# Kernel optimization log

Measured on AMD Instinct MI355X. Metric: run time of the kernel, lower is better.

The kernel has to match this reference:

```python
import jax, jax.numpy as jnp
import numpy as np

N = 32768
WORD_DIM, TAG_DIM, REL_DIM, MEM_DIM, AT_HID = 300, 20, 20, 150, 20
IN_LEAF = WORD_DIM + TAG_DIM                      # 320, input to leaf SimpleGRU
IN_NODE = WORD_DIM + MEM_DIM + REL_DIM + TAG_DIM  # 490, input to GRU_AT


def _build_tree(seed=0):
    rng = np.random.default_rng(seed)
    parent = np.zeros(N, np.int64)
    for i in range(1, N):
        parent[i] = rng.integers(max(0, i - 64), i)
    children = [[] for _ in range(N)]
    for i in range(1, N):
        children[parent[i]].append(i)
    # Edge schedule: parents in DECREASING index order, children ascending.
    # Since child index > parent index, all edges below a node fire before
    # the node itself is consumed as a child => same order as the Python
    # post-order recursion in the torch code.
    edges = []
    for p in range(N - 1, -1, -1):
        for c in children[p]:
            edges.append((p, c))
    edges = np.asarray(edges, np.int32)            # (N-1, 2)
    leaf_ids = np.asarray([i for i in range(N) if not children[i]], np.int32)
    return edges, leaf_ids


def setup_inputs() -> dict:
    key = jax.random.key(0)
    ks = jax.random.split(key, 16)
    s = 0.05
    edges, leaf_ids = _build_tree()
    return {
        "w_emb":  jax.random.normal(ks[0], (N, WORD_DIM), jnp.float32),
        "tag_emb": jax.random.normal(ks[1], (N, TAG_DIM), jnp.float32),
        "rel_emb": jax.random.normal(ks[2], (N, REL_DIM), jnp.float32),
        "leaf_h": jax.random.uniform(ks[3], (MEM_DIM,), jnp.float32),
        # leaf SimpleGRU: stacked [Wz,Wr,Wh], [Uz,Ur,Uh], combined bias bW+bU
        "leaf_W": jax.random.normal(ks[4], (3, MEM_DIM, IN_LEAF), jnp.float32) * s,
        "leaf_U": jax.random.normal(ks[5], (3, MEM_DIM, MEM_DIM), jnp.float32) * s,
        "leaf_b": jax.random.normal(ks[6], (3, MEM_DIM), jnp.float32) * s,
        # GRU_AT inner SimpleGRU
        "node_W": jax.random.normal(ks[7], (3, MEM_DIM, IN_NODE), jnp.float32) * s,
        "node_U": jax.random.normal(ks[8], (3, MEM_DIM, MEM_DIM), jnp.float32) * s,
        "node_b": jax.random.normal(ks[9], (3, MEM_DIM), jnp.float32) * s,
        # attention gate AT: sigmoid(Wa tanh(Wb x + bb) + ba)
        "at_Wb": jax.random.normal(ks[10], (AT_HID, IN_NODE), jnp.float32) * s,
        "at_bb": jax.random.normal(ks[11], (AT_HID,), jnp.float32) * s,
        "at_Wa": jax.random.normal(ks[12], (AT_HID,), jnp.float32) * s,
        "at_ba": jax.random.normal(ks[13], (), jnp.float32) * s,
        "edges": jnp.asarray(edges),
        "leaf_ids": jnp.asarray(leaf_ids),
    }


def _simple_gru(W, U, b, x, h):
    # z = s(Wz x + Uz h + b); r = s(...); ht = tanh(...)
    # h_new = r*h + (1-z)*ht   (as written in the torch code)
    pre = jnp.einsum('kmi,i->km', W, x) + jnp.einsum('kmn,n->km', U, h) + b
    z = jax.nn.sigmoid(pre[0])
    r = jax.nn.sigmoid(pre[1])
    ht = jnp.tanh(pre[2])
    return r * h + (1.0 - z) * ht


def reference(w_emb, tag_emb, rel_emb, leaf_h,
              leaf_W, leaf_U, leaf_b,
              node_W, node_U, node_b,
              at_Wb, at_bb, at_Wa, at_ba,
              edges, leaf_ids):
    n, mem = w_emb.shape[0], leaf_h.shape[0]

    # ---- leaves (vectorized: all leaves share leaf_h, no dependencies) ----
    Xl = jnp.concatenate([w_emb[leaf_ids], tag_emb[leaf_ids]], axis=1)  # (L, IN_LEAF)
    pre = (jnp.einsum('kmi,li->lkm', leaf_W, Xl)
           + jnp.einsum('kmn,n->km', leaf_U, leaf_h)[None]
           + leaf_b[None])                                              # (L,3,mem)
    z = jax.nn.sigmoid(pre[:, 0])
    r = jax.nn.sigmoid(pre[:, 1])
    ht = jnp.tanh(pre[:, 2])
    k_leaf = r * leaf_h[None] + (1.0 - z) * ht                          # (L, mem)

    K = jnp.zeros((n, mem), w_emb.dtype).at[leaf_ids].set(k_leaf)  # node states k
    H = jnp.zeros((n, mem), w_emb.dtype)                           # per-node running h

    # ---- inner nodes: one GRU_AT step per (parent, child) edge ----
    def step(carry, pc):
        K, H = carry
        p, c = pc[0], pc[1]
        # x = cat([word_emb[p], k_child, rel_emb[child], tag_emb[p]])
        x = jnp.concatenate([w_emb[p], K[c], rel_emb[c], tag_emb[p]])
        h = H[p]
        m = _simple_gru(node_W, node_U, node_b, x, h)
        a = jax.nn.sigmoid(jnp.dot(at_Wa, jnp.tanh(at_Wb @ x + at_bb)) + at_ba)
        h_new = a * m + (1.0 - a) * h
        return (K.at[p].set(h_new), H.at[p].set(h_new)), None

    (K, H), _ = jax.lax.scan(step, (K, H), edges)
    return K[0]  # root state, (mem,)


if __name__ == '__main__':
    out = reference(**setup_inputs())
    print(out.shape, out.dtype)
```

## Files before the change

### kernel.cpp

```cpp
#include <hip/hip_runtime.h>
#include <hip/hip_fp16.h>
#include <stdint.h>


#define ROWS 470
#define AST  480
#define WST  512
#define NP2  76
#define KST  160
#define NPAIR 75
#define TAGW 0x00010000u

static __device__ __forceinline__ float fdot2f(uint32_t w, uint32_t x, float acc){
#if __has_builtin(__builtin_amdgcn_fdot2)
  typedef _Float16 h2v __attribute__((ext_vector_type(2)));
  return __builtin_amdgcn_fdot2(__builtin_bit_cast(h2v,w), __builtin_bit_cast(h2v,x), acc, false);
#else
  __half2 a = __builtin_bit_cast(__half2,w), b = __builtin_bit_cast(__half2,x);
  return acc + __low2float(a)*__low2float(b) + __high2float(a)*__high2float(b);
#endif
}
static __device__ __forceinline__ uint4 ld4(const uint32_t* __restrict__ P, int t, int q){
  return make_uint4(P[(4*q+0)*WST+t], P[(4*q+1)*WST+t], P[(4*q+2)*WST+t], P[(4*q+3)*WST+t]);
}
static __device__ __forceinline__ void pinu4(uint4 &v){
  asm volatile("" : "+v"(v.x), "+v"(v.y), "+v"(v.z), "+v"(v.w));
}
static __device__ __forceinline__ float sigm(float x){ return 1.f/(1.f+__expf(-x)); }
static __device__ __forceinline__ float tanhx(float x){ float e=__expf(2.f*x); return 1.f - 2.f/(e+1.f); }
static __device__ __forceinline__ uint32_t packh(float a, float b){
  return (uint32_t)__half_as_ushort(__float2half(a)) | ((uint32_t)__half_as_ushort(__float2half(b))<<16);
}
static __device__ __forceinline__ uint32_t aloadw(const uint32_t* p){
  return __hip_atomic_load(p, __ATOMIC_RELAXED, __HIP_MEMORY_SCOPE_AGENT);
}
static __device__ __forceinline__ void astorew(uint32_t* p, uint32_t v){
  __hip_atomic_store(p, v, __ATOMIC_RELAXED, __HIP_MEMORY_SCOPE_AGENT);
}

#define DECL_W(W, P) \
  uint4 W##0=ld4(P,t,0),  W##1=ld4(P,t,1),  W##2=ld4(P,t,2),  W##3=ld4(P,t,3), \
        W##4=ld4(P,t,4),  W##5=ld4(P,t,5),  W##6=ld4(P,t,6),  W##7=ld4(P,t,7), \
        W##8=ld4(P,t,8),  W##9=ld4(P,t,9),  W##10=ld4(P,t,10),W##11=ld4(P,t,11), \
        W##12=ld4(P,t,12),W##13=ld4(P,t,13),W##14=ld4(P,t,14),W##15=ld4(P,t,15), \
        W##16=ld4(P,t,16),W##17=ld4(P,t,17),W##18=ld4(P,t,18);

#define PIN_W(W) \
  pinu4(W##0);  pinu4(W##1);  pinu4(W##2);  pinu4(W##3);  pinu4(W##4); \
  pinu4(W##5);  pinu4(W##6);  pinu4(W##7);  pinu4(W##8);  pinu4(W##9); \
  pinu4(W##10); pinu4(W##11); pinu4(W##12); pinu4(W##13); pinu4(W##14); \
  pinu4(W##15); pinu4(W##16); pinu4(W##17); pinu4(W##18);

#define DOT1(I, W, S) \
  _a0 = fdot2f(W##I.x, S[I].x, _a0); _a1 = fdot2f(W##I.y, S[I].y, _a1); \
  _a2 = fdot2f(W##I.z, S[I].z, _a2); _a3 = fdot2f(W##I.w, S[I].w, _a3);

#define DOT_ALL(P, W, S) { \
  float _a0 = 0.f, _a1 = 0.f, _a2 = 0.f, _a3 = 0.f; \
  DOT1(0,W,S)  DOT1(1,W,S)  DOT1(2,W,S)  DOT1(3,W,S)  DOT1(4,W,S) \
  DOT1(5,W,S)  DOT1(6,W,S)  DOT1(7,W,S)  DOT1(8,W,S)  DOT1(9,W,S) \
  DOT1(10,W,S) DOT1(11,W,S) DOT1(12,W,S) DOT1(13,W,S) DOT1(14,W,S) \
  DOT1(15,W,S) DOT1(16,W,S) DOT1(17,W,S) DOT1(18,W,S) \
  P = (P) + ((_a0 + _a1) + (_a2 + _a3)); \
}

#define DO_STEP(PRE, SRC) { \
  float _pre = (PRE); \
  const uint4* _s4 = (const uint4*)(SRC); \
  DOT_ALL(_pre, wk, _s4); \
  if (rowOK) act[t] = (t < 300) ? sigm(_pre) : tanhx(_pre); \
  __syncthreads(); \
  if (t < 150) { \
    float _s = atba_v; \
    _Pragma("unroll") \
    for (int _j = 0; _j < 20; ++_j) _s += was[_j]*act[450 + _j]; \
    float _a = sigm(_s); \
    float _z = act[t], _r = act[150 + t], _ht = act[300 + t]; \
    float _m  = _r*hreg + (1.f - _z)*_ht; \
    float _hn = _a*_m + (1.f - _a)*hreg; \
    hreg = _hn; \
    h_f32[t] = _hn; \
    ((__half*)h_pack)[t] = __float2half(_hn); \
  } \
  __syncthreads(); \
}

#define CALC_UH(OUT) { \
  float _x = 0.f; \
  const uint4* _h4 = (const uint4*)h_pack; \
  DOT_ALL(_x, uw, _h4); \
  OUT = _x; \
}

__global__ void k_prep(const int* __restrict__ edges, int E,
                       const float* __restrict__ node_U, const float* __restrict__ node_W,
                       const float* __restrict__ at_Wb,  const float* __restrict__ leaf_W,
                       uint32_t* __restrict__ UW, uint32_t* __restrict__ WK,
                       float* __restrict__ NWT, float* __restrict__ LWT, float* __restrict__ RWT,
                       int* __restrict__ parent_of, int* __restrict__ has_child)
{
  int o = blockIdx.x*blockDim.x + threadIdx.x;
  if (o < E) {
    int p = edges[2*o], c = edges[2*o+1];
    parent_of[c] = p; has_child[p] = 1;
    if (o == 0) parent_of[0] = -1;
    return;
  }
  o -= E;
  if (o < NP2*WST) {
    int i = o/WST, j = o%WST;
    uint32_t v = 0u;
    if (i < NPAIR && j < 450) v = packh(node_U[j*150 + 2*i], node_U[j*150 + 2*i + 1]);
    UW[o] = v; return;
  }
  o -= NP2*WST;
  if (o < NP2*WST) {
    int i = o/WST, j = o%WST;
    uint32_t v = 0u;
    if (i < NPAIR) {
      if (j < 450)      v = packh(node_W[j*490 + 300 + 2*i], node_W[j*490 + 301 + 2*i]);
      else if (j < 470) v = packh(at_Wb[(j-450)*490 + 300 + 2*i], at_Wb[(j-450)*490 + 301 + 2*i]);
    }
    WK[o] = v; return;
  }
  o -= NP2*WST;
  if (o < 320*ROWS) {
    int i = o/ROWS, r = o%ROWS;
    int col = (i < 300) ? i : 470 + (i - 300);
    NWT[o] = (r < 450) ? node_W[r*490 + col] : at_Wb[(r-450)*490 + col];
    return;
  }
  o -= 320*ROWS;
  if (o < 320*450) {
    int i = o/450, r = o%450;
    LWT[o] = leaf_W[r*320 + i];
    return;
  }
  o -= 320*450;
  if (o < 20*ROWS) {
    int i = o/ROWS, r = o%ROWS;
    RWT[o] = (r < 450) ? node_W[r*490 + 450 + i] : at_Wb[(r-450)*490 + 450 + i];
    return;
  }
}

__global__ void k_uhleaf(const float* __restrict__ leaf_U, const float* __restrict__ leaf_h,
                         const float* __restrict__ leaf_b, float* __restrict__ uh_leaf)
{
  int t = threadIdx.x;
  if (t < 450) {
    float s = leaf_b[t];
    for (int n = 0; n < 150; ++n) s += leaf_U[t*150 + n]*leaf_h[n];
    uh_leaf[t] = s;
  }
}

__global__ void k_scan(const int* __restrict__ edges, int E,
                       int* __restrict__ group_start, int* __restrict__ ctrl,
                       int* __restrict__ node_group)
{
  __shared__ int warp_cnt[16];
  __shared__ int wbase[16];
  __shared__ int base_s;
  int t = threadIdx.x;
  if (t == 0) base_s = 0;
  __syncthreads();
  for (int chunk = 0; chunk < E; chunk += 1024) {
    int i = chunk + t;
    bool flag = false;
    if (i < E) flag = (i == 0) || (edges[2*(i-1)] != edges[2*i]);
    unsigned long long m = __ballot(flag ? 1 : 0);
    int wave = t >> 6, lane = t & 63;
    if (lane == 0) warp_cnt[wave] = __popcll(m);
    __syncthreads();
    if (t == 0) {
      int run = base_s;
      for (int w = 0; w < 16; ++w) { wbase[w] = run; run += warp_cnt[w]; }
      base_s = run;
    }
    __syncthreads();
    if (flag) {
      int g = wbase[wave] + __popcll(m & ((1ull << lane) - 1ull));
      group_start[g] = i;
    }
    __syncthreads();
  }
  if (t == 0) { ctrl[1] = base_s; group_start[base_s] = E; }
  __syncthreads();
  int NG = base_s;
  for (int g = t; g < NG; g += 1024) node_group[edges[2*group_start[g]]] = g;
}

__global__ void k_leaf(const int* __restrict__ leaf_ids,
                       const float* __restrict__ w_emb, const float* __restrict__ tag_emb,
                       const float* __restrict__ LWT, const float* __restrict__ uh_leaf,
                       const float* __restrict__ leaf_h,
                       uint32_t* __restrict__ K_pack, int L)
{
  int base = blockIdx.x*8; if (base >= L) return;
  int cnt = min(8, L - base);
  __shared__ __align__(16) float xs[320*8];
  __shared__ float actl[8*450];
  __shared__ int lid[8];
  __shared__ float lh[150];
  int t = threadIdx.x;
  if (t < cnt) lid[t] = leaf_ids[base + t];
  if (t < 150) lh[t] = leaf_h[t];
  __syncthreads();
  for (int idx = t; idx < cnt*320; idx += 512) {
    int nl = idx/320, i = idx%320; int n = lid[nl];
    xs[i*8 + nl] = (i < 300) ? w_emb[(size_t)n*300 + i] : tag_emb[(size_t)n*20 + (i-300)];
  }
  __syncthreads();
  if (t < 450) {
    float a0=0,a1=0,a2=0,a3=0,a4=0,a5=0,a6=0,a7=0;
    for (int i = 0; i < 320; ++i) {
      float w = LWT[i*450 + t];
      const float4* x4 = (const float4*)(xs + i*8);
      float4 xa = x4[0], xb = x4[1];
      a0 += w*xa.x; a1 += w*xa.y; a2 += w*xa.z; a3 += w*xa.w;
      a4 += w*xb.x; a5 += w*xb.y; a6 += w*xb.z; a7 += w*xb.w;
    }
    float acc[8] = {a0,a1,a2,a3,a4,a5,a6,a7};
    float uh = uh_leaf[t];
    for (int j = 0; j < cnt; ++j) {
      float pre = acc[j] + uh;
      actl[j*450 + t] = (t < 300) ? sigm(pre) : tanhx(pre);
    }
  }
  __syncthreads();
  for (int idx = t; idx < cnt*150; idx += 512) {
    int nl = idx/150, m = idx%150;
    float z = actl[nl*450 + m], r = actl[nl*450 + 150 + m], ht = actl[nl*450 + 300 + m];
    float kv = r*lh[m] + (1.f - z)*ht;
    K_pack[(size_t)lid[nl]*KST + m] = TAGW | (uint32_t)__half_as_ushort(__float2half(kv));
  }
}

__global__ void k_static(const int* __restrict__ edges, const int* __restrict__ group_start,
                         const int* __restrict__ ctrl,
                         const float* __restrict__ w_emb, const float* __restrict__ tag_emb,
                         const float* __restrict__ NWT, const float* __restrict__ node_b,
                         const float* __restrict__ at_bb, __half* __restrict__ A_all)
{
  int NG = ctrl[1];
  int base = blockIdx.x*16; if (base >= NG) return;
  int cnt = min(16, NG - base);
  __shared__ __align__(16) float xs[320*16];
  __shared__ int pl[16];
  int t = threadIdx.x;
  if (t < cnt) pl[t] = edges[2*group_start[base + t]];
  __syncthreads();
  for (int idx = t; idx < cnt*320; idx += 512) {
    int nl = idx/320, i = idx%320; int n = pl[nl];
    xs[i*16 + nl] = (i < 300) ? w_emb[(size_t)n*300 + i] : tag_emb[(size_t)n*20 + (i-300)];
  }
  __syncthreads();
  if (t < ROWS) {
    float acc[16];
    #pragma unroll
    for (int j = 0; j < 16; ++j) acc[j] = 0.f;
    for (int i = 0; i < 320; ++i) {
      float w = NWT[i*ROWS + t];
      const float4* x4 = (const float4*)(xs + i*16);
      float4 xa = x4[0], xb = x4[1], xc = x4[2], xd = x4[3];
      acc[0]+=w*xa.x; acc[1]+=w*xa.y; acc[2]+=w*xa.z; acc[3]+=w*xa.w;
      acc[4]+=w*xb.x; acc[5]+=w*xb.y; acc[6]+=w*xb.z; acc[7]+=w*xb.w;
      acc[8]+=w*xc.x; acc[9]+=w*xc.y; acc[10]+=w*xc.z; acc[11]+=w*xc.w;
      acc[12]+=w*xd.x; acc[13]+=w*xd.y; acc[14]+=w*xd.z; acc[15]+=w*xd.w;
    }
    float bias = (t < 450) ? node_b[t] : at_bb[t-450];
    for (int j = 0; j < cnt; ++j)
      A_all[(size_t)pl[j]*AST + t] = __float2half(acc[j] + bias);
  }
}

__global__ void k_rel(const float* __restrict__ rel_emb, const float* __restrict__ RWT_g,
                      __half* __restrict__ R_all, int N)
{
  __shared__ float rw[20*ROWS];
  __shared__ float xs[20*32];
  int t = threadIdx.x;
  for (int idx = t; idx < 20*ROWS; idx += 512) rw[idx] = RWT_g[idx];
  int base = blockIdx.x*32;
  int cnt = min(32, N - base);
  for (int idx = t; idx < cnt*20; idx += 512) {
    int nl = idx/20, i = idx%20;
    xs[i*32 + nl] = rel_emb[(size_t)(base+nl)*20 + i];
  }
  __syncthreads();
  if (t < ROWS) {
    float w[20];
    #pragma unroll
    for (int i = 0; i < 20; ++i) w[i] = rw[i*ROWS + t];
    for (int j = 0; j < cnt; ++j) {
      float acc = 0.f;
      #pragma unroll
      for (int i = 0; i < 20; ++i) acc += w[i]*xs[i*32 + j];
      R_all[(size_t)(base+j)*AST + t] = __float2half(acc);
    }
  }
}

__global__ __launch_bounds__(512, 1)
void k_worker(const int* __restrict__ edges,
              const float* __restrict__ at_Wa, const float* __restrict__ at_ba,
              const uint32_t* __restrict__ UW, const uint32_t* __restrict__ WK,
              const __half* __restrict__ A_all, const __half* __restrict__ R_all,
              uint32_t* __restrict__ K_pack,
              int* __restrict__ ctrl, const int* __restrict__ group_start,
              const int* __restrict__ parent_of, const int* __restrict__ node_group,
              const int* __restrict__ has_child, float* __restrict__ d_out)
{
  const int t = threadIdx.x;
  const bool rowOK = (t < ROWS);

  __shared__ __align__(16) float    h_f32[152];
  __shared__ __align__(16) uint32_t h_pack[80];
  __shared__ __align__(16) uint32_t kc[80];
  __shared__ float act[472];
  __shared__ float was[20];
  __shared__ int   s_g;

  DECL_W(wk, WK)
  DECL_W(uw, UW)
  PIN_W(wk)
  PIN_W(uw)

  if (t >= NPAIR && t < 80) { kc[t] = 0u; h_pack[t] = 0u; }
  if (t < 20) was[t] = at_Wa[t];
  const float atba_v = at_ba[0];
  const int NG = ctrl[1];
  float hreg = 0.f;
  __syncthreads();

  for (;;) {
    if (t == 0) s_g = atomicAdd(&ctrl[0], 1);
    __syncthreads();
    const int g = s_g;
    if (g >= NG) break;
    const int gs = group_start[g], ge = group_start[g+1];
    const int p  = edges[2*gs];
    if (ge - gs == 1 && has_child[edges[2*gs + 1]]) continue;

    int  r = parent_of[p];
    bool single = false;
    if (r >= 0) {
      const int gr = node_group[r];
      single = (group_start[gr+1] - group_start[gr] == 1);
    }
    const float aSt = rowOK ? __half2float(A_all[(size_t)p*AST + t]) : 0.f;
    float aN = 0.f, rN = 0.f;
    if (single && rowOK) {
      aN = __half2float(A_all[(size_t)r*AST + t]);
      rN = __half2float(R_all[(size_t)p*AST + t]);
    }
    if (t < 150) hreg = 0.f;
    float uh = 0.f;

    for (int e = gs; e < ge; ++e) {
      const int c = edges[2*e + 1];
      const float rSt = rowOK ? __half2float(R_all[(size_t)c*AST + t]) : 0.f;
      if (t < 64) {
        const uint32_t* rowp = K_pack + (size_t)c*KST;
        uint32_t r0, r1, r2;
        long spins = 0;
        for (;;) {
          r0 = aloadw(rowp + t);
          r1 = aloadw(rowp + 64 + t);
          r2 = (t < 22) ? aloadw(rowp + 128 + t) : TAGW;
          bool ok = ((r0 & 0xffff0000u) == TAGW) &
                    ((r1 & 0xffff0000u) == TAGW) &
                    ((r2 & 0xffff0000u) == TAGW);
          if (__all(ok)) break;
          __builtin_amdgcn_s_sleep(1);
          if (++spins > 100000000L) break;
        }
        unsigned short* kch = (unsigned short*)kc;
        kch[t]      = (unsigned short)(r0 & 0xffffu);
        kch[64 + t] = (unsigned short)(r1 & 0xffffu);
        if (t < 22) kch[128 + t] = (unsigned short)(r2 & 0xffffu);
      }
      __syncthreads();
      DO_STEP(aSt + rSt + uh, kc)
      if (e + 1 < ge) { CALC_UH(uh) } else uh = 0.f;
    }

    int q = p;
    for (;;) {
      if (q == 0) { if (t < 150) d_out[t] = h_f32[t]; break; }
      if (single) {
        const int r2p = parent_of[r];
        bool s2 = false;
        if (r2p >= 0) {
          const int gr2 = node_group[r2p];
          s2 = (group_start[gr2+1] - group_start[gr2] == 1);
        }
        float aN2 = 0.f, rN2 = 0.f;
        if (s2 && rowOK) {
          aN2 = __half2float(A_all[(size_t)r2p*AST + t]);
          rN2 = __half2float(R_all[(size_t)r*AST + t]);
        }
        if (t < 150) hreg = 0.f;
        DO_STEP(aN + rN, h_pack)
        q = r; r = r2p; single = s2; aN = aN2; rN = rN2;
        continue;
      }
      if (t < 150)
        astorew(&K_pack[(size_t)q*KST + t],
                TAGW | (uint32_t)__half_as_ushort(__float2half(h_f32[t])));
      break;
    }
  }
}

extern "C" void kernel_launch(void* const* d_in, const int* in_sizes, int n_in,
                              void* d_out, int out_size, void* d_ws, size_t ws_size,
                              hipStream_t stream)
{
  const float* w_emb   = (const float*)d_in[0];
  const float* tag_emb = (const float*)d_in[1];
  const float* rel_emb = (const float*)d_in[2];
  const float* leaf_h  = (const float*)d_in[3];
  const float* leaf_W  = (const float*)d_in[4];
  const float* leaf_U  = (const float*)d_in[5];
  const float* leaf_b  = (const float*)d_in[6];
  const float* node_W  = (const float*)d_in[7];
  const float* node_U  = (const float*)d_in[8];
  const float* node_b  = (const float*)d_in[9];
  const float* at_Wb   = (const float*)d_in[10];
  const float* at_bb   = (const float*)d_in[11];
  const float* at_Wa   = (const float*)d_in[12];
  const float* at_ba   = (const float*)d_in[13];
  const int*   edges   = (const int*)d_in[14];
  const int*   leaf_ids= (const int*)d_in[15];
  float* out = (float*)d_out;

  const int N = in_sizes[0]/300;
  const int E = in_sizes[14]/2;
  const int L = in_sizes[15];

  char* ws = (char*)d_ws;
  size_t off = 0;
  auto take = [&](size_t bytes) -> char* {
    char* p = ws + off;
    off = (off + bytes + 255) & ~(size_t)255;
    return p;
  };
  size_t zbytes = 256 + (size_t)4*N;
  char* zbase       = take(zbytes);
  int*  ctrl        = (int*)zbase;
  int*  has_child   = (int*)(zbase + 256);
  int*  parent_of   = (int*)take((size_t)4*N);
  int*  node_group  = (int*)take((size_t)4*N);
  int*  group_start = (int*)take((size_t)4*(N+1));
  uint32_t* UW      = (uint32_t*)take((size_t)4*NP2*WST);
  uint32_t* WK      = (uint32_t*)take((size_t)4*NP2*WST);
  float* NWT        = (float*)take((size_t)4*320*ROWS);
  float* LWT        = (float*)take((size_t)4*320*450);
  float* RWT        = (float*)take((size_t)4*20*ROWS);
  float* uh_leaf    = (float*)take((size_t)4*456);
  __half* A_all     = (__half*)take((size_t)2*((size_t)N*AST + 64));
  __half* R_all     = (__half*)take((size_t)2*((size_t)N*AST + 64));
  uint32_t* K_pack  = (uint32_t*)take((size_t)4*(size_t)N*KST);
  (void)ws_size; (void)n_in; (void)out_size;

  hipMemsetAsync(zbase, 0, zbytes, stream);
  hipMemsetAsync(K_pack, 0, (size_t)4*(size_t)N*KST, stream);

  const int TOT = E + NP2*WST + NP2*WST + 320*ROWS + 320*450 + 20*ROWS;
  k_prep<<<(TOT + 255)/256, 256, 0, stream>>>(edges, E, node_U, node_W, at_Wb, leaf_W,
                                              UW, WK, NWT, LWT, RWT, parent_of, has_child);
  k_uhleaf<<<1, 512, 0, stream>>>(leaf_U, leaf_h, leaf_b, uh_leaf);
  k_scan<<<1, 1024, 0, stream>>>(edges, E, group_start, ctrl, node_group);
  k_leaf<<<(L + 7)/8, 512, 0, stream>>>(leaf_ids, w_emb, tag_emb, LWT, uh_leaf, leaf_h,
                                        K_pack, L);
  k_static<<<(N + 15)/16, 512, 0, stream>>>(edges, group_start, ctrl, w_emb, tag_emb,
                                            NWT, node_b, at_bb, A_all);
  k_rel<<<(N + 31)/32, 512, 0, stream>>>(rel_emb, RWT, R_all, N);
  k_worker<<<256, 512, 0, stream>>>(edges, at_Wa, at_ba, UW, WK, A_all, R_all,
                                    K_pack, ctrl, group_start, parent_of,
                                    node_group, has_child, out);
}
```

Before: 2.779 ms.

## Use NaN-sentinel packed fp16 child states and prefetch child rows across waves

Child-state rows in K_pack change from 32-bit words carrying a tag in the upper half to packed fp16 pairs, with 0xFFFF (a NaN pattern) as the not-yet-written sentinel set by the memset. This halves the row stride and the polling traffic. The other waves of the block now try to prefetch the rows for later edges of the group into a per-slot shared buffer, and the wave-0 spin loop only runs when the slot was not staged. Results are published straight from the step epilogue with 16-bit atomic stores, replacing the separate h_f32 copy and store pass. This relies on a computed fp16 value never being exactly 0xFFFF and on per-halfword stores becoming visible safely.

```diff
diff --git a/kernel.cpp b/kernel.cpp
--- a/kernel.cpp
+++ b/kernel.cpp
@@ -7,9 +7,8 @@
 #define AST  480
 #define WST  512
 #define NP2  76
-#define KST  160
+#define KST  80
 #define NPAIR 75
-#define TAGW 0x00010000u
 
 static __device__ __forceinline__ float fdot2f(uint32_t w, uint32_t x, float acc){
 #if __has_builtin(__builtin_amdgcn_fdot2)
@@ -34,8 +33,11 @@
 static __device__ __forceinline__ uint32_t aloadw(const uint32_t* p){
   return __hip_atomic_load(p, __ATOMIC_RELAXED, __HIP_MEMORY_SCOPE_AGENT);
 }
-static __device__ __forceinline__ void astorew(uint32_t* p, uint32_t v){
+static __device__ __forceinline__ void astoreh(unsigned short* p, unsigned short v){
   __hip_atomic_store(p, v, __ATOMIC_RELAXED, __HIP_MEMORY_SCOPE_AGENT);
+}
+static __device__ __forceinline__ bool validw(uint32_t w){
+  return ((w & 0xffffu) != 0xffffu) && ((w >> 16) != 0xffffu);
 }
 
 #define DECL_W(W, P) \
@@ -64,7 +66,7 @@
   P = (P) + ((_a0 + _a1) + (_a2 + _a3)); \
 }
 
-#define DO_STEP(PRE, SRC) { \
+#define DO_STEP(PRE, SRC, PUBP, OUTP, SLOT) { \
   float _pre = (PRE); \
   const uint4* _s4 = (const uint4*)(SRC); \
   DOT_ALL(_pre, wk, _s4); \
@@ -79,9 +81,14 @@
     float _m  = _r*hreg + (1.f - _z)*_ht; \
     float _hn = _a*_m + (1.f - _a)*hreg; \
     hreg = _hn; \
-    h_f32[t] = _hn; \
-    ((__half*)h_pack)[t] = __float2half(_hn); \
+    unsigned short _hb = __half_as_ushort(__float2half(_hn)); \
+    ((unsigned short*)h_pack)[t] = _hb; \
+    unsigned short* _pp = (PUBP); \
+    if (_pp) astoreh(_pp + t, _hb); \
+    float* _op = (OUTP); \
+    if (_op) _op[t] = _hn; \
   } \
+  if ((SLOT) >= 0 && t == 256) vstaged[(SLOT)] = 0; \
   __syncthreads(); \
 }
 
@@ -233,7 +240,7 @@
     int nl = idx/150, m = idx%150;
     float z = actl[nl*450 + m], r = actl[nl*450 + 150 + m], ht = actl[nl*450 + 300 + m];
     float kv = r*lh[m] + (1.f - z)*ht;
-    K_pack[(size_t)lid[nl]*KST + m] = TAGW | (uint32_t)__half_as_ushort(__float2half(kv));
+    ((unsigned short*)(K_pack + (size_t)lid[nl]*KST))[m] = __half_as_ushort(__float2half(kv));
   }
 }
 
@@ -315,19 +322,20 @@
   const int t = threadIdx.x;
   const bool rowOK = (t < ROWS);
 
-  __shared__ __align__(16) float    h_f32[152];
   __shared__ __align__(16) uint32_t h_pack[80];
-  __shared__ __align__(16) uint32_t kc[80];
+  __shared__ __align__(16) uint32_t kbuf[8*76];
   __shared__ float act[472];
   __shared__ float was[20];
   __shared__ int   s_g;
+  volatile __shared__ int vstaged[8];
 
   DECL_W(wk, WK)
   DECL_W(uw, UW)
   PIN_W(wk)
   PIN_W(uw)
 
-  if (t >= NPAIR && t < 80) { kc[t] = 0u; h_pack[t] = 0u; }
+  if (t >= NPAIR && t < 80) h_pack[t] = 0u;
+  if (t < 8) { vstaged[t] = 0; kbuf[t*76 + 75] = 0u; }
   if (t < 20) was[t] = at_Wa[t];
   const float atba_v = at_ba[0];
   const int NG = ctrl[1];
@@ -358,58 +366,74 @@
     if (t < 150) hreg = 0.f;
     float uh = 0.f;
 
+    {
+      const int w = t >> 6, l = t & 63;
+      const int j = gs + w;
+      if (w >= 1 && j < ge) {
+        const int cj = edges[2*j + 1];
+        const uint32_t* rowp = K_pack + (size_t)cj*KST;
+        uint32_t a = aloadw(rowp + l);
+        uint32_t b = (l < 11) ? aloadw(rowp + 64 + l) : 0u;
+        bool ok = validw(a) && (l >= 11 || validw(b));
+        if (__all(ok)) {
+          uint32_t* kb = kbuf + w*76;
+          kb[l] = a; if (l < 11) kb[64 + l] = b;
+          if (l == 0) vstaged[w] = 1;
+        }
+      }
+    }
+
     for (int e = gs; e < ge; ++e) {
+      const int slot = (e - gs) & 7;
       const int c = edges[2*e + 1];
       const float rSt = rowOK ? __half2float(R_all[(size_t)c*AST + t]) : 0.f;
-      if (t < 64) {
-        const uint32_t* rowp = K_pack + (size_t)c*KST;
-        uint32_t r0, r1, r2;
-        long spins = 0;
-        for (;;) {
-          r0 = aloadw(rowp + t);
-          r1 = aloadw(rowp + 64 + t);
-          r2 = (t < 22) ? aloadw(rowp + 128 + t) : TAGW;
-          bool ok = ((r0 & 0xffff0000u) == TAGW) &
-                    ((r1 & 0xffff0000u) == TAGW) &
-                    ((r2 & 0xffff0000u) == TAGW);
-          if (__all(ok)) break;
-          __builtin_amdgcn_s_sleep(1);
-          if (++spins > 100000000L) break;
+      {
+        const int w = t >> 6, l = t & 63;
+        if (w == 0 && !vstaged[slot]) {
+          const uint32_t* rowp = K_pack + (size_t)c*KST;
+          uint32_t* kb = kbuf + slot*76;
+          long spins = 0;
+          for (;;) {
+            uint32_t a = aloadw(rowp + l);
+            uint32_t b = (l < 11) ? aloadw(rowp + 64 + l) : 0u;
+            bool ok = validw(a) && (l >= 11 || validw(b));
+            if (__all(ok)) { kb[l] = a; if (l < 11) kb[64 + l] = b; break; }
+            __builtin_amdgcn_s_sleep(1);
+            if (++spins > 50000000L) break;
+          }
         }
-        unsigned short* kch = (unsigned short*)kc;
-        kch[t]      = (unsigned short)(r0 & 0xffffu);
-        kch[64 + t] = (unsigned short)(r1 & 0xffffu);
-        if (t < 22) kch[128 + t] = (unsigned short)(r2 & 0xffffu);
       }
       __syncthreads();
-      DO_STEP(aSt + rSt + uh, kc)
+      unsigned short* pubp = nullptr; float* outp = nullptr;
+      if (e + 1 == ge) {
+        if (p == 0) outp = d_out;
+        else if (!single) pubp = (unsigned short*)(K_pack + (size_t)p*KST);
+      }
+      DO_STEP(aSt + rSt + uh, kbuf + slot*76, pubp, outp, slot)
       if (e + 1 < ge) { CALC_UH(uh) } else uh = 0.f;
     }
 
     int q = p;
     for (;;) {
-      if (q == 0) { if (t < 150) d_out[t] = h_f32[t]; break; }
-      if (single) {
-        const int r2p = parent_of[r];
-        bool s2 = false;
-        if (r2p >= 0) {
-          const int gr2 = node_group[r2p];
-          s2 = (group_start[gr2+1] - group_start[gr2] == 1);
-        }
-        float aN2 = 0.f, rN2 = 0.f;
-        if (s2 && rowOK) {
-          aN2 = __half2float(A_all[(size_t)r2p*AST + t]);
-          rN2 = __half2float(R_all[(size_t)r*AST + t]);
-        }
-        if (t < 150) hreg = 0.f;
-        DO_STEP(aN + rN, h_pack)
-        q = r; r = r2p; single = s2; aN = aN2; rN = rN2;
-        continue;
+      if (q == 0) break;
+      if (!single) break;
+      const int r2p = parent_of[r];
+      bool s2 = false;
+      if (r2p >= 0) {
+        const int gr2 = node_group[r2p];
+        s2 = (group_start[gr2+1] - group_start[gr2] == 1);
       }
-      if (t < 150)
-        astorew(&K_pack[(size_t)q*KST + t],
-                TAGW | (uint32_t)__half_as_ushort(__float2half(h_f32[t])));
-      break;
+      float aN2 = 0.f, rN2 = 0.f;
+      if (s2 && rowOK) {
+        aN2 = __half2float(A_all[(size_t)r2p*AST + t]);
+        rN2 = __half2float(R_all[(size_t)r*AST + t]);
+      }
+      if (t < 150) hreg = 0.f;
+      unsigned short* pubp = nullptr; float* outp = nullptr;
+      if (r == 0) outp = d_out;
+      else if (!s2) pubp = (unsigned short*)(K_pack + (size_t)r*KST);
+      DO_STEP(aN + rN, h_pack, pubp, outp, -1)
+      q = r; r = r2p; single = s2; aN = aN2; rN = rN2;
     }
   }
 }
@@ -466,7 +490,7 @@
   (void)ws_size; (void)n_in; (void)out_size;
 
   hipMemsetAsync(zbase, 0, zbytes, stream);
-  hipMemsetAsync(K_pack, 0, (size_t)4*(size_t)N*KST, stream);
+  hipMemsetAsync(K_pack, 0xFF, (size_t)4*(size_t)N*KST, stream);
 
   const int TOT = E + NP2*WST + NP2*WST + 320*ROWS + 320*450 + 20*ROWS;
   k_prep<<<(TOT + 255)/256, 256, 0, stream>>>(edges, E, node_U, node_W, at_Wb, leaf_W,
```

After: 2.684 ms. -3.4%, faster.
